# Performance work log

Hardware: AMD Instinct MI355X
Metric: run time of the kernel (lower is better)

## Reference

```python
import jax, jax.numpy as jnp
import numpy as np

B, L, C = 1, 1536, 768
H, DK, DV, F = 8, 64, 96, 96


def setup_inputs() -> dict:
    key = jax.random.key(0)
    ks = jax.random.split(key, 9)
    s = 0.02
    return {
        "x": jax.random.normal(ks[0], (B, L, C), jnp.float32),
        "Wq": jax.random.normal(ks[1], (C, H * DK), jnp.float32) * s,
        "Wk": jax.random.normal(ks[2], (C, H * DK), jnp.float32) * s,
        "Wv": jax.random.normal(ks[3], (C, H * DV), jnp.float32) * s,
        "Wout": jax.random.normal(ks[4], (H * DV, C), jnp.float32) * s,
        "bout": jnp.zeros((C,), jnp.float32),
        "Wpos": jax.random.normal(ks[5], (F, H * DK), jnp.float32) * s,
        "rel_content_bias": jax.random.normal(ks[6], (1, H, 1, DK), jnp.float32),
        "rel_pos_bias": jax.random.normal(ks[7], (1, H, 1, DK), jnp.float32),
    }


def central_mask_embed(n, features):
    # positions: -(n-1) .. n-1  -> (2n-1,)
    positions = jnp.arange(-(n - 1), n)
    # center widths: 2^1 - 1 .. 2^features - 1
    widths = jnp.float32(2.0) ** jnp.arange(1, features + 1, dtype=jnp.float32) - 1.0
    return (widths[None, :] > jnp.abs(positions).astype(jnp.float32)[:, None]).astype(jnp.float32)


def relative_shift(t):
    # t: (b, h, t1, t2) with t2 = 2*t1 - 1 -> (b, h, t1, t1)
    b, h, t1, t2 = t.shape
    t = jnp.pad(t, ((0, 0), (0, 0), (0, 0), (1, 0)))  # (b,h,t1,t2+1)
    t = t.reshape(b, h, t2 + 1, t1)[:, :, 1:, :]       # (b,h,t2,t1)
    t = t.reshape(b, h, t1, t2)
    return t[..., : (t2 + 2) // 2]


def reference(x, Wq, Wk, Wv, Wout, bout, Wpos, rel_content_bias, rel_pos_bias):
    b, n, _ = x.shape
    q = (x @ Wq).reshape(b, n, H, DK).transpose(0, 2, 1, 3)  # b h n d
    k = (x @ Wk).reshape(b, n, H, DK).transpose(0, 2, 1, 3)
    v = (x @ Wv).reshape(b, n, H, DV).transpose(0, 2, 1, 3)
    q = q / jnp.float32(DK) ** 0.5

    content_logits = jnp.einsum("bhid,bhjd->bhij", q + rel_content_bias, k)

    pos = central_mask_embed(n, F)                 # (2n-1, F)
    pos_k = (pos @ Wpos).reshape(2 * n - 1, H, DK).transpose(1, 0, 2)  # h (2n-1) d
    pos_logits = jnp.einsum("bhid,hjd->bhij", q + rel_pos_bias, pos_k)
    pos_logits = relative_shift(pos_logits)        # (b,h,n,n)

    attn = jax.nn.softmax(content_logits + pos_logits, axis=-1)
    out = jnp.einsum("bhij,bhjd->bhid", attn, v)   # b h n dv
    out = out.transpose(0, 2, 1, 3).reshape(b, n, H * DV)
    return out @ Wout + bout
```

## Files before the change

### kernel.cpp

```cpp
#include <hip/hip_runtime.h>
#include <stdint.h>

#define NTOK 1536
#define CDIM 768
#define NH 8
#define DKH 64
#define DVH 96
#define NF 96

typedef unsigned short u16;
typedef __attribute__((ext_vector_type(8))) short s16x8;
typedef __attribute__((ext_vector_type(4))) float f32x4;

#define LGKM0() asm volatile("s_waitcnt lgkmcnt(0)" ::: "memory")

__device__ __forceinline__ float b2f(u16 u) {
    union { uint32_t i; float f; } v; v.i = ((uint32_t)u) << 16; return v.f;
}
__device__ __forceinline__ u16 f2b(float f) {
    union { float f; uint32_t i; } v; v.f = f;
    uint32_t x = v.i;
    return (u16)((x + 0x7FFFu + ((x >> 16) & 1u)) >> 16);
}
__device__ __forceinline__ float ldin(const void* p, int i, int f32) {
    return f32 ? ((const float*)p)[i] : b2f(((const u16*)p)[i]);
}

#define FIDX(m, kk) ((((kk) >> 3) * 16 + (m)) * 8 + ((kk) & 7))

#define OFF_WSUF 16
#define OFF_S11  (OFF_WSUF + 5632)
#define OFF_QF   (OFF_S11 + 147456)
#define OFF_KF   (OFF_QF + 393216)
#define OFF_VF   (OFF_KF + 393216)
#define OFF_AOF  (OFF_VF + 589824)
#define OFF_XF   (OFF_AOF + 589824)
#define OFF_WF   (OFF_XF + 589824)
#define OFF_WOF  (OFF_WF + 688128)

struct In9 { const void* p[9]; int n[9]; };

__global__ __launch_bounds__(256) void probe_all(In9 s, int* __restrict__ flags) {
    __shared__ int bad;
    int k = blockIdx.x;
    if (threadIdx.x == 0) bad = 0;
    __syncthreads();
    const u16* a = (const u16*)s.p[k];
    int n = s.n[k];
    if (n > 2048) n = 2048;
    int my = 0;
    for (int i = threadIdx.x; i < n; i += 256) {
        float v = b2f(a[i]);
        if (!(fabsf(v) < 1e6f)) my = 1;
    }
    if (my) atomicOr(&bad, 1);
    __syncthreads();
    if (threadIdx.x == 0) flags[k] = bad;
}

__global__ __launch_bounds__(256) void prep(const void* __restrict__ x,
                                            const void* __restrict__ Wq,
                                            const void* __restrict__ Wk,
                                            const void* __restrict__ Wv,
                                            const void* __restrict__ Wout,
                                            const void* __restrict__ Wpos,
                                            int fx, int fq, int fk, int fv,
                                            int fw, int fpos,
                                            float* __restrict__ ws) {
    const int* flags = (const int*)ws;
    int bx = blockIdx.x, tid = threadIdx.x;
    int wv = tid >> 6, L = tid & 63;

    if (bx < 144) {
        int f = flags[fx];
        u16* dst = (u16*)(ws + OFF_XF);
        int cbase = (bx * 4 + wv) * 4;
        int m = L & 15, kq = L >> 4;
        int srcs[4];
#pragma unroll
        for (int c = 0; c < 4; ++c) {
            int ch = cbase + c;
            int ti = ch / 24, kc = ch % 24;
            srcs[c] = (ti * 16 + m) * CDIM + kc * 32 + kq * 8;
        }
        if (f) {
            float4 a[4][2];
#pragma unroll
            for (int c = 0; c < 4; ++c) {
                const float* xp = (const float*)x + srcs[c];
                a[c][0] = *(const float4*)(xp);
                a[c][1] = *(const float4*)(xp + 4);
            }
#pragma unroll
            for (int c = 0; c < 4; ++c) {
                union { u16 u[8]; uint4 v; } pk;
                pk.u[0] = f2b(a[c][0].x); pk.u[1] = f2b(a[c][0].y);
                pk.u[2] = f2b(a[c][0].z); pk.u[3] = f2b(a[c][0].w);
                pk.u[4] = f2b(a[c][1].x); pk.u[5] = f2b(a[c][1].y);
                pk.u[6] = f2b(a[c][1].z); pk.u[7] = f2b(a[c][1].w);
                *(uint4*)(dst + (cbase + c) * 512 + L * 8) = pk.v;
            }
        } else {
            uint4 v[4];
#pragma unroll
            for (int c = 0; c < 4; ++c) v[c] = *(const uint4*)((const u16*)x + srcs[c]);
#pragma unroll
            for (int c = 0; c < 4; ++c)
                *(uint4*)(dst + (cbase + c) * 512 + L * 8) = v[c];
        }
        return;
    }
    if (bx < 1104) {
        int c = (bx - 144) * 4 + wv;
        const void* src; int ld, cn0, f; u16* dst; int kc;
        if (c < 2688) {
            int tn = c / 24; kc = c % 24;
            int n0 = tn * 16;
            dst = (u16*)(ws + OFF_WF) + c * 512;
            if (n0 < 512)       { src = Wq; ld = 512;  cn0 = n0;        f = flags[fq]; }
            else if (n0 < 1024) { src = Wk; ld = 512;  cn0 = n0 - 512;  f = flags[fk]; }
            else                { src = Wv; ld = CDIM; cn0 = n0 - 1024; f = flags[fv]; }
        } else {
            int c2 = c - 2688;
            int tn = c2 / 24; kc = c2 % 24;
            dst = (u16*)(ws + OFF_WOF) + c2 * 512;
            src = Wout; ld = CDIM; cn0 = tn * 16; f = flags[fw];
        }
        int nn = L & 15, kq = L >> 4;
        int base = (kc * 32 + kq * 8) * ld + cn0 + nn;
        union { u16 u[8]; uint4 v; } pk;
        if (f) {
            const float* sp = (const float*)src + base;
            float a0 = sp[0], a1 = sp[ld], a2 = sp[2 * ld], a3 = sp[3 * ld];
            float a4 = sp[4 * ld], a5 = sp[5 * ld], a6 = sp[6 * ld], a7 = sp[7 * ld];
            pk.u[0] = f2b(a0); pk.u[1] = f2b(a1); pk.u[2] = f2b(a2); pk.u[3] = f2b(a3);
            pk.u[4] = f2b(a4); pk.u[5] = f2b(a5); pk.u[6] = f2b(a6); pk.u[7] = f2b(a7);
        } else {
            const u16* sp = (const u16*)src + base;
            pk.u[0] = sp[0]; pk.u[1] = sp[ld]; pk.u[2] = sp[2 * ld]; pk.u[3] = sp[3 * ld];
            pk.u[4] = sp[4 * ld]; pk.u[5] = sp[5 * ld]; pk.u[6] = sp[6 * ld]; pk.u[7] = sp[7 * ld];
        }
        *(uint4*)(dst + L * 8) = pk.v;
        return;
    }
    int t = bx - 1104;
    int f = flags[fpos];
    for (int hd = tid; hd < 512; hd += 256) {
        float s0 = 0.f, s1 = 0.f, s2 = 0.f, s3 = 0.f;
        int f0 = t;
        for (; f0 + 4 <= NF; f0 += 4) {
            s0 += ldin(Wpos, f0 * 512 + hd, f);
            s1 += ldin(Wpos, (f0 + 1) * 512 + hd, f);
            s2 += ldin(Wpos, (f0 + 2) * 512 + hd, f);
            s3 += ldin(Wpos, (f0 + 3) * 512 + hd, f);
        }
        for (; f0 < NF; ++f0) s0 += ldin(Wpos, f0 * 512 + hd, f);
        ws[OFF_WSUF + t * 512 + hd] = (s0 + s1) + (s2 + s3);
    }
}

__global__ __launch_bounds__(256) void qkv_reg(const void* __restrict__ rcb,
                                               const void* __restrict__ rpb,
                                               int fc, int fp,
                                               float* __restrict__ ws) {
    __shared__ float qt[64 * 68];
    __shared__ float rpd[12];
    const int* flags = (const int*)ws;
    const u16* xf = (const u16*)(ws + OFF_XF);
    const u16* wf = (const u16*)(ws + OFF_WF);
    u16* qf = (u16*)(ws + OFF_QF);
    u16* kf = (u16*)(ws + OFF_KF);
    u16* vf = (u16*)(ws + OFF_VF);

    int tid = threadIdx.x;
    int lane = tid & 63, w = tid >> 6;
    int quad = lane >> 4, col = lane & 15;
    int ti4 = blockIdx.x;
    int tn4 = blockIdx.y;
    int tn = tn4 * 4 + w;
    int i0 = ti4 * 64;
    bool isQ = (tn4 < 8);
    int hq = tn4;

    if (isQ && tid < 12) {
        float s = 0.f;
        if (tid < 11) {
            const float* wp = ws + OFF_WSUF + tid * 512 + hq * 64;
            int f32p = flags[fp];
            for (int d = 0; d < 64; ++d) s += ldin(rpb, hq * 64 + d, f32p) * wp[d];
        }
        rpd[tid] = s;
    }

    f32x4 acc[4];
#pragma unroll
    for (int mt = 0; mt < 4; ++mt) acc[mt] = (f32x4){0.f, 0.f, 0.f, 0.f};

    const u16* bp = wf + (tn * 24) * 512 + lane * 8;
    const u16* ap = xf + (ti4 * 4 * 24) * 512 + lane * 8;
#pragma unroll 4
    for (int kc = 0; kc < 24; ++kc) {
        s16x8 bfrag = *(const s16x8*)(bp + kc * 512);
#pragma unroll
        for (int mt = 0; mt < 4; ++mt) {
            s16x8 afrag = *(const s16x8*)(ap + (mt * 24 + kc) * 512);
            acc[mt] = __builtin_amdgcn_mfma_f32_16x16x32_bf16(afrag, bfrag, acc[mt], 0, 0, 0);
        }
    }

    if (isQ) {
#pragma unroll
        for (int mt = 0; mt < 4; ++mt)
#pragma unroll
            for (int r = 0; r < 4; ++r)
                qt[(mt * 16 + quad * 4 + r) * 68 + w * 16 + col] = acc[mt][r] * 0.125f;
        __syncthreads();
        int f32c = flags[fc];
        for (int idx = tid; idx < 64 * 64; idx += 256) {
            int row = idx >> 6, d = idx & 63;
            int ti = ti4 * 4 + (row >> 4), m = row & 15;
            u16 val = f2b(qt[row * 68 + d] + ldin(rcb, hq * 64 + d, f32c));
            qf[((hq * 96 + ti) * 2 + (d >> 5)) * 512 + FIDX(m, d & 31)] = val;
        }
        const float* wsuf = ws + OFF_WSUF;
        float* s11 = ws + OFF_S11;
        for (int idx = tid; idx < 64 * 12; idx += 256) {
            int row = idx / 12, t = idx % 12;
            float s = rpd[t];
            if (t < 11) {
                const float* wp = wsuf + t * 512 + hq * 64;
                const float* qr = qt + row * 68;
                for (int d = 0; d < 64; ++d) s += qr[d] * wp[d];
            }
            s11[(hq * NTOK + i0 + row) * 12 + t] = s;
        }
    } else if (tn < 64) {
        int h = (tn >> 2) - 8;
        int d = ((tn & 3) * 16) + col;
#pragma unroll
        for (int mt = 0; mt < 4; ++mt) {
            int tj = ti4 * 4 + mt;
#pragma unroll
            for (int r = 0; r < 4; ++r) {
                int nn = quad * 4 + r;
                kf[((h * 96 + tj) * 2 + (d >> 5)) * 512 + FIDX(nn, d & 31)] = f2b(acc[mt][r]);
            }
        }
    } else {
        int c = tn * 16 + col - 1024;
        int h = c / 96, d = c % 96;
        int nt = d >> 4, nn = d & 15;
#pragma unroll
        for (int mt = 0; mt < 4; ++mt) {
#pragma unroll
            for (int r = 0; r < 4; ++r) {
                int j = i0 + mt * 16 + quad * 4 + r;
                int jc = j >> 5, kk = j & 31;
                vf[((h * 48 + jc) * 6 + nt) * 512 + FIDX(nn, kk)] = f2b(acc[mt][r]);
            }
        }
    }
}

__global__ __launch_bounds__(256) void attn_mfma(float* __restrict__ ws) {
    __shared__ float s11b[192];
    __shared__ alignas(16) u16 pbuf[4][2][16 * 36];
    __shared__ float Om[4][16 * 96];
    __shared__ float lw[4][16];

    const u16* qf = (const u16*)(ws + OFF_QF);
    const u16* kf = (const u16*)(ws + OFF_KF);
    const u16* vf = (const u16*)(ws + OFF_VF);
    const float* s11 = ws + OFF_S11;
    u16* aof = (u16*)(ws + OFF_AOF);

    int h = blockIdx.x & 7;
    int ti = blockIdx.x >> 3;
    int i0 = ti * 16;
    int tid = threadIdx.x;
    int wv = tid >> 6, lane = tid & 63;
    int quad = lane >> 4, col = lane & 15;

    if (tid < 192) s11b[tid] = s11[(h * NTOK + i0 + tid / 12) * 12 + tid % 12];
    const u16* qp = qf + ((h * 96 + ti) * 2) * 512 + lane * 8;
    s16x8 a_lo = *(const s16x8*)(qp);
    s16x8 a_hi = *(const s16x8*)(qp + 512);
    __syncthreads();

    f32x4 O[2][6];
    float lsum[4];
#pragma unroll
    for (int s = 0; s < 2; ++s)
#pragma unroll
        for (int nt = 0; nt < 6; ++nt) O[s][nt] = (f32x4){0.f, 0.f, 0.f, 0.f};
#pragma unroll
    for (int r = 0; r < 4; ++r) lsum[r] = 0.f;

    for (int c = 0; c < 6; ++c) {
        f32x4 S[2][2];
#pragma unroll
        for (int s = 0; s < 2; ++s) {
            int tj0 = wv * 24 + s * 12 + c * 2;
            const u16* kp = kf + ((h * 96 + tj0) * 2) * 512 + lane * 8;
            s16x8 b0lo = *(const s16x8*)(kp);
            s16x8 b0hi = *(const s16x8*)(kp + 512);
            s16x8 b1lo = *(const s16x8*)(kp + 1024);
            s16x8 b1hi = *(const s16x8*)(kp + 1536);
            f32x4 t0 = (f32x4){0.f, 0.f, 0.f, 0.f};
            f32x4 t1 = (f32x4){0.f, 0.f, 0.f, 0.f};
            t0 = __builtin_amdgcn_mfma_f32_16x16x32_bf16(a_lo, b0lo, t0, 0, 0, 0);
            t0 = __builtin_amdgcn_mfma_f32_16x16x32_bf16(a_hi, b0hi, t0, 0, 0, 0);
            t1 = __builtin_amdgcn_mfma_f32_16x16x32_bf16(a_lo, b1lo, t1, 0, 0, 0);
            t1 = __builtin_amdgcn_mfma_f32_16x16x32_bf16(a_hi, b1hi, t1, 0, 0, 0);
            S[s][0] = t0; S[s][1] = t1;
        }
        LGKM0();
#pragma unroll
        for (int s = 0; s < 2; ++s) {
            int j0 = wv * 384 + s * 192 + c * 32;
            int lo1 = j0 - (i0 + 15), lo2 = i0 - (j0 + 31);
            int dmin = lo1 > 0 ? lo1 : (lo2 > 0 ? lo2 : 0);
            int dm1 = i0 + 15 - j0, dm2 = j0 + 31 - i0;
            int dmax = dm1 > dm2 ? dm1 : dm2;
            int tlo = 31 - __builtin_clz(dmin + 1);
            int thi = 31 - __builtin_clz(dmax + 1);
            if (tlo == thi) {
#pragma unroll
                for (int r = 0; r < 4; ++r) {
                    int row = quad * 4 + r;
                    float bv = s11b[row * 12 + tlo] - 12.f;
                    float p0 = __expf(S[s][0][r] + bv);
                    float p1 = __expf(S[s][1][r] + bv);
                    pbuf[wv][s][row * 36 + col] = f2b(p0);
                    pbuf[wv][s][row * 36 + 16 + col] = f2b(p1);
                    lsum[r] += p0 + p1;
                }
            } else {
#pragma unroll
                for (int r = 0; r < 4; ++r) {
                    int row = quad * 4 + r;
                    int ig = i0 + row;
                    int d0 = ig - (j0 + col); d0 = d0 < 0 ? -d0 : d0;
                    int d1 = ig - (j0 + 16 + col); d1 = d1 < 0 ? -d1 : d1;
                    float v0 = S[s][0][r] + s11b[row * 12 + (31 - __builtin_clz(d0 + 1))];
                    float v1 = S[s][1][r] + s11b[row * 12 + (31 - __builtin_clz(d1 + 1))];
                    float p0 = __expf(v0 - 12.f);
                    float p1 = __expf(v1 - 12.f);
                    pbuf[wv][s][row * 36 + col] = f2b(p0);
                    pbuf[wv][s][row * 36 + 16 + col] = f2b(p1);
                    lsum[r] += p0 + p1;
                }
            }
        }
        LGKM0();
#pragma unroll
        for (int s = 0; s < 2; ++s) {
            int jc = wv * 12 + s * 6 + c;
            const u16* pr = &pbuf[wv][s][col * 36 + quad * 8];
            union { s16x8 v; uint2 u2[2]; } pa;
            pa.u2[0] = *(const uint2*)(pr);
            pa.u2[1] = *(const uint2*)(pr + 4);
            const u16* vp = vf + ((h * 48 + jc) * 6) * 512 + lane * 8;
#pragma unroll
            for (int nt = 0; nt < 6; ++nt) {
                s16x8 vfr = *(const s16x8*)(vp + nt * 512);
                O[s][nt] = __builtin_amdgcn_mfma_f32_16x16x32_bf16(pa.v, vfr, O[s][nt], 0, 0, 0);
            }
        }
    }

#pragma unroll
    for (int off = 1; off < 16; off <<= 1)
#pragma unroll
        for (int r = 0; r < 4; ++r) lsum[r] += __shfl_xor(lsum[r], off);
    if (col == 0)
#pragma unroll
        for (int r = 0; r < 4; ++r) lw[wv][quad * 4 + r] = lsum[r];
#pragma unroll
    for (int r = 0; r < 4; ++r) {
        int row = quad * 4 + r;
#pragma unroll
        for (int nt = 0; nt < 6; ++nt)
            Om[wv][row * 96 + nt * 16 + col] = O[0][nt][r] + O[1][nt][r];
    }
    __syncthreads();
    for (int idx = tid; idx < 16 * 96; idx += 256) {
        int row = idx / 96, cc = idx % 96;
        float L = lw[0][row] + lw[1][row] + lw[2][row] + lw[3][row];
        float val = (Om[0][idx] + Om[1][idx] + Om[2][idx] + Om[3][idx]) / L;
        aof[(ti * 24 + h * 3 + (cc >> 5)) * 512 + FIDX(row, cc & 31)] = f2b(val);
    }
}

__global__ __launch_bounds__(256) void out_reg(const void* __restrict__ bout,
                                               int fb,
                                               float* __restrict__ ws,
                                               float* __restrict__ out) {
    const int* flags = (const int*)ws;
    const u16* af = (const u16*)(ws + OFF_AOF);
    const u16* wof = (const u16*)(ws + OFF_WOF);
    int f32b = flags[fb];

    int tid = threadIdx.x;
    int lane = tid & 63, w = tid >> 6;
    int quad = lane >> 4, col = lane & 15;
    int ti4 = blockIdx.x;
    int tn = blockIdx.y * 4 + w;
    int i0 = ti4 * 64;
    int n0 = blockIdx.y * 64;

    f32x4 acc[4];
#pragma unroll
    for (int mt = 0; mt < 4; ++mt) acc[mt] = (f32x4){0.f, 0.f, 0.f, 0.f};

    const u16* bp = wof + (tn * 24) * 512 + lane * 8;
    const u16* ap = af + (ti4 * 4 * 24) * 512 + lane * 8;
#pragma unroll 4
    for (int kc = 0; kc < 24; ++kc) {
        s16x8 bfrag = *(const s16x8*)(bp + kc * 512);
#pragma unroll
        for (int mt = 0; mt < 4; ++mt) {
            s16x8 afrag = *(const s16x8*)(ap + (mt * 24 + kc) * 512);
            acc[mt] = __builtin_amdgcn_mfma_f32_16x16x32_bf16(afrag, bfrag, acc[mt], 0, 0, 0);
        }
    }

    int c = n0 + w * 16 + col;
    float bias = ldin(bout, c, f32b);
#pragma unroll
    for (int mt = 0; mt < 4; ++mt) {
#pragma unroll
        for (int r = 0; r < 4; ++r) {
            int i = i0 + mt * 16 + quad * 4 + r;
            out[i * CDIM + c] = acc[mt][r] + bias;
        }
    }
}

extern "C" void kernel_launch(void* const* d_in, const int* in_sizes, int n_in,
                              void* d_out, int out_size, void* d_ws, size_t ws_size,
                              hipStream_t stream) {
    float* out = (float*)d_out;
    float* ws = (float*)d_ws;

    const int want[9] = {1179648, 393216, 393216, 589824, 589824, 768, 49152, 512, 512};
    int role2in[9], used[9] = {0};
    bool ok = (n_in == 9);
    if (ok) {
        for (int r = 0; r < 9; ++r) {
            int found = -1;
            for (int i = 0; i < 9 && found < 0; ++i)
                if (!used[i] && in_sizes[i] == want[r]) found = i;
            if (found < 0) { ok = false; break; }
            used[found] = 1;
            role2in[r] = found;
        }
    }
    if (!ok) for (int r = 0; r < 9; ++r) role2in[r] = r;

    const void* x    = d_in[role2in[0]];
    const void* Wq   = d_in[role2in[1]];
    const void* Wk   = d_in[role2in[2]];
    const void* Wv   = d_in[role2in[3]];
    const void* Wout = d_in[role2in[4]];
    const void* bout = d_in[role2in[5]];
    const void* Wpos = d_in[role2in[6]];
    const void* rcb  = d_in[role2in[7]];
    const void* rpb  = d_in[role2in[8]];

    In9 s;
    for (int i = 0; i < 9; ++i) { s.p[i] = d_in[i]; s.n[i] = in_sizes[i]; }
    hipLaunchKernelGGL(probe_all, dim3(9), dim3(256), 0, stream, s, (int*)ws);

    hipLaunchKernelGGL(prep, dim3(1115), dim3(256), 0, stream,
                       x, Wq, Wk, Wv, Wout, Wpos,
                       role2in[0], role2in[1], role2in[2], role2in[3],
                       role2in[4], role2in[6], ws);
    hipLaunchKernelGGL(qkv_reg, dim3(24, 28), dim3(256), 0, stream,
                       rcb, rpb, role2in[7], role2in[8], ws);
    hipLaunchKernelGGL(attn_mfma, dim3(768), dim3(256), 0, stream, ws);
    hipLaunchKernelGGL(out_reg, dim3(24, 12), dim3(256), 0, stream,
                       bout, role2in[5], ws, out);
}
```

Before: 158.2 us.

## Use MFMA for s11 bias projection and split attention across eight waves

In qkv_reg, the scalar per-row dot products that build the s11 position-bias table are replaced by two bf16 MFMA ops against a packed weight fragment. The Q store is also rewritten as vectorized 16-byte fragment writes. attn_mfma now launches 512 threads per block, so each of eight waves owns one key segment instead of four waves each handling two, and the final reduction sums eight partials. The aim is to cut scalar FMA work and raise wave-level parallelism, at the cost of bf16 rounding in s11 and more shared memory and reduction work per block.

```diff
diff --git a/kernel.cpp b/kernel.cpp
--- a/kernel.cpp
+++ b/kernel.cpp
@@ -182,14 +182,29 @@
     bool isQ = (tn4 < 8);
     int hq = tn4;
 
-    if (isQ && tid < 12) {
-        float s = 0.f;
-        if (tid < 11) {
-            const float* wp = ws + OFF_WSUF + tid * 512 + hq * 64;
-            int f32p = flags[fp];
-            for (int d = 0; d < 64; ++d) s += ldin(rpb, hq * 64 + d, f32p) * wp[d];
-        }
-        rpd[tid] = s;
+    s16x8 bw0, bw1;
+    if (isQ) {
+        int t = lane & 15, kq = lane >> 4;
+        union { u16 u[8]; s16x8 v; } p0, p1;
+#pragma unroll
+        for (int j = 0; j < 8; ++j) {
+            float v0 = 0.f, v1 = 0.f;
+            if (t < 11) {
+                v0 = ws[OFF_WSUF + t * 512 + hq * 64 + kq * 8 + j];
+                v1 = ws[OFF_WSUF + t * 512 + hq * 64 + 32 + kq * 8 + j];
+            }
+            p0.u[j] = f2b(v0); p1.u[j] = f2b(v1);
+        }
+        bw0 = p0.v; bw1 = p1.v;
+        if (tid < 12) {
+            float s = 0.f;
+            if (tid < 11) {
+                const float* wp = ws + OFF_WSUF + tid * 512 + hq * 64;
+                int f32p = flags[fp];
+                for (int d = 0; d < 64; ++d) s += ldin(rpb, hq * 64 + d, f32p) * wp[d];
+            }
+            rpd[tid] = s;
+        }
     }
 
     f32x4 acc[4];
@@ -216,23 +231,32 @@
                 qt[(mt * 16 + quad * 4 + r) * 68 + w * 16 + col] = acc[mt][r] * 0.125f;
         __syncthreads();
         int f32c = flags[fc];
-        for (int idx = tid; idx < 64 * 64; idx += 256) {
-            int row = idx >> 6, d = idx & 63;
-            int ti = ti4 * 4 + (row >> 4), m = row & 15;
-            u16 val = f2b(qt[row * 68 + d] + ldin(rcb, hq * 64 + d, f32c));
-            qf[((hq * 96 + ti) * 2 + (d >> 5)) * 512 + FIDX(m, d & 31)] = val;
-        }
-        const float* wsuf = ws + OFF_WSUF;
-        float* s11 = ws + OFF_S11;
-        for (int idx = tid; idx < 64 * 12; idx += 256) {
-            int row = idx / 12, t = idx % 12;
-            float s = rpd[t];
-            if (t < 11) {
-                const float* wp = wsuf + t * 512 + hq * 64;
-                const float* qr = qt + row * 68;
-                for (int d = 0; d < 64; ++d) s += qr[d] * wp[d];
-            }
-            s11[(hq * NTOK + i0 + row) * 12 + t] = s;
+        int m = lane & 15, kq = lane >> 4;
+#pragma unroll
+        for (int kc2 = 0; kc2 < 2; ++kc2) {
+            union { u16 u[8]; uint4 v; } pk;
+#pragma unroll
+            for (int j = 0; j < 8; ++j) {
+                int d = kc2 * 32 + kq * 8 + j;
+                pk.u[j] = f2b(qt[(w * 16 + m) * 68 + d] + ldin(rcb, hq * 64 + d, f32c));
+            }
+            *(uint4*)(qf + (((hq * 96 + ti4 * 4 + w) * 2 + kc2) * 512) + lane * 8) = pk.v;
+        }
+        union { u16 u[8]; s16x8 v; } qa0, qa1;
+#pragma unroll
+        for (int j = 0; j < 8; ++j) {
+            qa0.u[j] = f2b(qt[(w * 16 + m) * 68 + kq * 8 + j]);
+            qa1.u[j] = f2b(qt[(w * 16 + m) * 68 + 32 + kq * 8 + j]);
+        }
+        f32x4 s11a = (f32x4){0.f, 0.f, 0.f, 0.f};
+        s11a = __builtin_amdgcn_mfma_f32_16x16x32_bf16(qa0.v, bw0, s11a, 0, 0, 0);
+        s11a = __builtin_amdgcn_mfma_f32_16x16x32_bf16(qa1.v, bw1, s11a, 0, 0, 0);
+        if (col < 12) {
+            float rp = rpd[col];
+            float* s11 = ws + OFF_S11;
+#pragma unroll
+            for (int r = 0; r < 4; ++r)
+                s11[(hq * NTOK + i0 + w * 16 + quad * 4 + r) * 12 + col] = s11a[r] + rp;
         }
     } else if (tn < 64) {
         int h = (tn >> 2) - 8;
@@ -262,11 +286,11 @@
     }
 }
 
-__global__ __launch_bounds__(256) void attn_mfma(float* __restrict__ ws) {
+__global__ __launch_bounds__(512) void attn_mfma(float* __restrict__ ws) {
     __shared__ float s11b[192];
-    __shared__ alignas(16) u16 pbuf[4][2][16 * 36];
-    __shared__ float Om[4][16 * 96];
-    __shared__ float lw[4][16];
+    __shared__ alignas(16) u16 pbuf[8][16 * 36];
+    __shared__ float Om[8][16 * 96];
+    __shared__ float lw[8][16];
 
     const u16* qf = (const u16*)(ws + OFF_QF);
     const u16* kf = (const u16*)(ws + OFF_KF);
@@ -287,85 +311,73 @@
     s16x8 a_hi = *(const s16x8*)(qp + 512);
     __syncthreads();
 
-    f32x4 O[2][6];
+    f32x4 O[6];
     float lsum[4];
 #pragma unroll
-    for (int s = 0; s < 2; ++s)
-#pragma unroll
-        for (int nt = 0; nt < 6; ++nt) O[s][nt] = (f32x4){0.f, 0.f, 0.f, 0.f};
+    for (int nt = 0; nt < 6; ++nt) O[nt] = (f32x4){0.f, 0.f, 0.f, 0.f};
 #pragma unroll
     for (int r = 0; r < 4; ++r) lsum[r] = 0.f;
 
     for (int c = 0; c < 6; ++c) {
-        f32x4 S[2][2];
-#pragma unroll
-        for (int s = 0; s < 2; ++s) {
-            int tj0 = wv * 24 + s * 12 + c * 2;
-            const u16* kp = kf + ((h * 96 + tj0) * 2) * 512 + lane * 8;
-            s16x8 b0lo = *(const s16x8*)(kp);
-            s16x8 b0hi = *(const s16x8*)(kp + 512);
-            s16x8 b1lo = *(const s16x8*)(kp + 1024);
-            s16x8 b1hi = *(const s16x8*)(kp + 1536);
-            f32x4 t0 = (f32x4){0.f, 0.f, 0.f, 0.f};
-            f32x4 t1 = (f32x4){0.f, 0.f, 0.f, 0.f};
-            t0 = __builtin_amdgcn_mfma_f32_16x16x32_bf16(a_lo, b0lo, t0, 0, 0, 0);
-            t0 = __builtin_amdgcn_mfma_f32_16x16x32_bf16(a_hi, b0hi, t0, 0, 0, 0);
-            t1 = __builtin_amdgcn_mfma_f32_16x16x32_bf16(a_lo, b1lo, t1, 0, 0, 0);
-            t1 = __builtin_amdgcn_mfma_f32_16x16x32_bf16(a_hi, b1hi, t1, 0, 0, 0);
-            S[s][0] = t0; S[s][1] = t1;
-        }
+        int tj0 = wv * 12 + c * 2;
+        const u16* kp = kf + ((h * 96 + tj0) * 2) * 512 + lane * 8;
+        s16x8 b0lo = *(const s16x8*)(kp);
+        s16x8 b0hi = *(const s16x8*)(kp + 512);
+        s16x8 b1lo = *(const s16x8*)(kp + 1024);
+        s16x8 b1hi = *(const s16x8*)(kp + 1536);
+        f32x4 t0 = (f32x4){0.f, 0.f, 0.f, 0.f};
+        f32x4 t1 = (f32x4){0.f, 0.f, 0.f, 0.f};
+        t0 = __builtin_amdgcn_mfma_f32_16x16x32_bf16(a_lo, b0lo, t0, 0, 0, 0);
+        t0 = __builtin_amdgcn_mfma_f32_16x16x32_bf16(a_hi, b0hi, t0, 0, 0, 0);
+        t1 = __builtin_amdgcn_mfma_f32_16x16x32_bf16(a_lo, b1lo, t1, 0, 0, 0);
+        t1 = __builtin_amdgcn_mfma_f32_16x16x32_bf16(a_hi, b1hi, t1, 0, 0, 0);
+
         LGKM0();
-#pragma unroll
-        for (int s = 0; s < 2; ++s) {
-            int j0 = wv * 384 + s * 192 + c * 32;
-            int lo1 = j0 - (i0 + 15), lo2 = i0 - (j0 + 31);
-            int dmin = lo1 > 0 ? lo1 : (lo2 > 0 ? lo2 : 0);
-            int dm1 = i0 + 15 - j0, dm2 = j0 + 31 - i0;
-            int dmax = dm1 > dm2 ? dm1 : dm2;
-            int tlo = 31 - __builtin_clz(dmin + 1);
-            int thi = 31 - __builtin_clz(dmax + 1);
-            if (tlo == thi) {
-#pragma unroll
-                for (int r = 0; r < 4; ++r) {
-                    int row = quad * 4 + r;
-                    float bv = s11b[row * 12 + tlo] - 12.f;
-                    float p0 = __expf(S[s][0][r] + bv);
-                    float p1 = __expf(S[s][1][r] + bv);
-                    pbuf[wv][s][row * 36 + col] = f2b(p0);
-                    pbuf[wv][s][row * 36 + 16 + col] = f2b(p1);
-                    lsum[r] += p0 + p1;
-                }
-            } else {
-#pragma unroll
-                for (int r = 0; r < 4; ++r) {
-                    int row = quad * 4 + r;
-                    int ig = i0 + row;
-                    int d0 = ig - (j0 + col); d0 = d0 < 0 ? -d0 : d0;
-                    int d1 = ig - (j0 + 16 + col); d1 = d1 < 0 ? -d1 : d1;
-                    float v0 = S[s][0][r] + s11b[row * 12 + (31 - __builtin_clz(d0 + 1))];
-                    float v1 = S[s][1][r] + s11b[row * 12 + (31 - __builtin_clz(d1 + 1))];
-                    float p0 = __expf(v0 - 12.f);
-                    float p1 = __expf(v1 - 12.f);
-                    pbuf[wv][s][row * 36 + col] = f2b(p0);
-                    pbuf[wv][s][row * 36 + 16 + col] = f2b(p1);
-                    lsum[r] += p0 + p1;
-                }
+        int j0 = wv * 192 + c * 32;
+        int lo1 = j0 - (i0 + 15), lo2 = i0 - (j0 + 31);
+        int dmin = lo1 > 0 ? lo1 : (lo2 > 0 ? lo2 : 0);
+        int dm1 = i0 + 15 - j0, dm2 = j0 + 31 - i0;
+        int dmax = dm1 > dm2 ? dm1 : dm2;
+        int tlo = 31 - __builtin_clz(dmin + 1);
+        int thi = 31 - __builtin_clz(dmax + 1);
+        if (tlo == thi) {
+#pragma unroll
+            for (int r = 0; r < 4; ++r) {
+                int row = quad * 4 + r;
+                float bv = s11b[row * 12 + tlo] - 12.f;
+                float p0 = __expf(t0[r] + bv);
+                float p1 = __expf(t1[r] + bv);
+                pbuf[wv][row * 36 + col] = f2b(p0);
+                pbuf[wv][row * 36 + 16 + col] = f2b(p1);
+                lsum[r] += p0 + p1;
+            }
+        } else {
+#pragma unroll
+            for (int r = 0; r < 4; ++r) {
+                int row = quad * 4 + r;
+                int ig = i0 + row;
+                int d0 = ig - (j0 + col); d0 = d0 < 0 ? -d0 : d0;
+                int d1 = ig - (j0 + 16 + col); d1 = d1 < 0 ? -d1 : d1;
+                float v0 = t0[r] + s11b[row * 12 + (31 - __builtin_clz(d0 + 1))];
+                float v1 = t1[r] + s11b[row * 12 + (31 - __builtin_clz(d1 + 1))];
+                float p0 = __expf(v0 - 12.f);
+                float p1 = __expf(v1 - 12.f);
+                pbuf[wv][row * 36 + col] = f2b(p0);
+                pbuf[wv][row * 36 + 16 + col] = f2b(p1);
+                lsum[r] += p0 + p1;
             }
         }
         LGKM0();
-#pragma unroll
-        for (int s = 0; s < 2; ++s) {
-            int jc = wv * 12 + s * 6 + c;
-            const u16* pr = &pbuf[wv][s][col * 36 + quad * 8];
-            union { s16x8 v; uint2 u2[2]; } pa;
-            pa.u2[0] = *(const uint2*)(pr);
-            pa.u2[1] = *(const uint2*)(pr + 4);
-            const u16* vp = vf + ((h * 48 + jc) * 6) * 512 + lane * 8;
-#pragma unroll
-            for (int nt = 0; nt < 6; ++nt) {
-                s16x8 vfr = *(const s16x8*)(vp + nt * 512);
-                O[s][nt] = __builtin_amdgcn_mfma_f32_16x16x32_bf16(pa.v, vfr, O[s][nt], 0, 0, 0);
-            }
+        int jc = wv * 6 + c;
+        const u16* pr = &pbuf[wv][col * 36 + quad * 8];
+        union { s16x8 v; uint2 u2[2]; } pa;
+        pa.u2[0] = *(const uint2*)(pr);
+        pa.u2[1] = *(const uint2*)(pr + 4);
+        const u16* vp = vf + ((h * 48 + jc) * 6) * 512 + lane * 8;
+#pragma unroll
+        for (int nt = 0; nt < 6; ++nt) {
+            s16x8 vfr = *(const s16x8*)(vp + nt * 512);
+            O[nt] = __builtin_amdgcn_mfma_f32_16x16x32_bf16(pa.v, vfr, O[nt], 0, 0, 0);
         }
     }
 
@@ -381,14 +393,15 @@
         int row = quad * 4 + r;
 #pragma unroll
         for (int nt = 0; nt < 6; ++nt)
-            Om[wv][row * 96 + nt * 16 + col] = O[0][nt][r] + O[1][nt][r];
+            Om[wv][row * 96 + nt * 16 + col] = O[nt][r];
     }
     __syncthreads();
-    for (int idx = tid; idx < 16 * 96; idx += 256) {
+    for (int idx = tid; idx < 16 * 96; idx += 512) {
         int row = idx / 96, cc = idx % 96;
-        float L = lw[0][row] + lw[1][row] + lw[2][row] + lw[3][row];
-        float val = (Om[0][idx] + Om[1][idx] + Om[2][idx] + Om[3][idx]) / L;
-        aof[(ti * 24 + h * 3 + (cc >> 5)) * 512 + FIDX(row, cc & 31)] = f2b(val);
+        float L = 0.f, val = 0.f;
+#pragma unroll
+        for (int v = 0; v < 8; ++v) { L += lw[v][row]; val += Om[v][idx]; }
+        aof[(ti * 24 + h * 3 + (cc >> 5)) * 512 + FIDX(row, cc & 31)] = f2b(val / L);
     }
 }
 
@@ -478,7 +491,7 @@
                        role2in[4], role2in[6], ws);
     hipLaunchKernelGGL(qkv_reg, dim3(24, 28), dim3(256), 0, stream,
                        rcb, rpb, role2in[7], role2in[8], ws);
-    hipLaunchKernelGGL(attn_mfma, dim3(768), dim3(256), 0, stream, ws);
+    hipLaunchKernelGGL(attn_mfma, dim3(768), dim3(512), 0, stream, ws);
     hipLaunchKernelGGL(out_reg, dim3(24, 12), dim3(256), 0, stream,
                        bout, role2in[5], ws, out);
 }
```

After: 151.3 us. -4.4%, faster.
